# Kernel tuning notes

Hardware: AMD Instinct MI355X
Metric: run time of the kernel (lower is better)

The kernel has to match this reference:

```python
import jax, jax.numpy as jnp
import numpy as np

B, N, L = 256, 4096, 6
EMBED, HID, VOCAB = 16, 32, 200
NOTE, LSTM_D, T = 64, 64, 128


def _tree_structure():
    """One random tree of N nodes (root=node 0), tiled across the batch.
    height = distance above deepest descendant; children have strictly smaller height."""
    rng = np.random.default_rng(0)
    height = np.zeros(N, np.int32)
    height[0] = L
    height[1:] = rng.integers(0, L, N - 1)
    kind = np.full(N, 2, np.int32)  # 2 = internal
    leaf_mask = height == 0
    kind[leaf_mask] = (rng.random(leaf_mask.sum()) < 0.1).astype(np.int32)  # 1=ptr, 0=leaf
    parent = np.zeros(N, np.int64)
    for hl in range(L):
        mask = height == hl
        cand = np.where((height > hl) & (kind == 2))[0]  # root always qualifies
        parent[mask] = rng.choice(cand, size=int(mask.sum()))
    parent[0] = 0  # root points to itself; harmless (its own h stays 0 until final level)
    return height, kind, parent


def setup_inputs():
    height, kind, parent = _tree_structure()
    offs = (np.arange(B, dtype=np.int64) * N)[:, None]
    rng = np.random.default_rng(1)
    inp = {
        'kind': jnp.asarray(np.tile(kind, B), jnp.int32),
        'height': jnp.asarray(np.tile(height, B), jnp.int32),
        'parent': jnp.asarray((parent[None, :] + offs).reshape(-1), jnp.int32),
        'tok_a': jnp.asarray(rng.integers(0, VOCAB, B * N), jnp.int32),
        'tok_b': jnp.asarray(rng.integers(0, VOCAB, B * N), jnp.int32),
        'ptr_time': jnp.asarray(rng.integers(0, T, B * N), jnp.int32),
    }
    key = jax.random.key(0)
    ks = jax.random.split(key, 16)
    def w(k, shape, scale=0.05):
        return (jax.random.normal(k, shape, jnp.float32) * scale)
    inp['first_notes'] = w(ks[0], (B, NOTE), 1.0)
    inp['lstm_out'] = w(ks[1], (B, T, LSTM_D), 1.0)
    inp['embedding'] = w(ks[2], (VOCAB, EMBED), 0.02)
    inp['leaf_w1'] = w(ks[3], (2 * EMBED, HID)); inp['leaf_b1'] = w(ks[4], (HID,))
    inp['leaf_w2'] = w(ks[5], (HID, HID));       inp['leaf_b2'] = w(ks[6], (HID,))
    inp['node_w'] = w(ks[7], (2 * EMBED + HID, HID)); inp['node_b'] = w(ks[8], (HID,))
    inp['ptr_w'] = w(ks[9], (NOTE + LSTM_D, HID));    inp['ptr_b'] = w(ks[10], (HID,))
    inp['ff_w1'] = w(ks[11], (HID, HID)); inp['ff_b1'] = w(ks[12], (HID,))
    inp['ff_w2'] = w(ks[13], (HID, HID)); inp['ff_b2'] = w(ks[14], (HID,))
    inp['tail_w'] = w(ks[15], (HID, 1)); inp['tail_b'] = jnp.zeros((1,), jnp.float32)
    return inp


def reference(kind, height, parent, tok_a, tok_b, ptr_time, first_notes, lstm_out,
              embedding, leaf_w1, leaf_b1, leaf_w2, leaf_b2, node_w, node_b,
              ptr_w, ptr_b, ff_w1, ff_b1, ff_w2, ff_b2, tail_w, tail_b):
    M = kind.shape[0]
    nb = first_notes.shape[0]
    n_per = M // nb
    tree_id = jnp.arange(M, dtype=jnp.int32) // n_per
    emb_a = embedding[tok_a]  # [M, EMBED] (parent-type / first-token embed)
    emb_b = embedding[tok_b]  # [M, EMBED] (node-type / second-token embed)
    pair = jnp.concatenate([emb_a, emb_b], axis=-1)  # [M, 2*EMBED]
    # leaf path: two stacked linears (no nonlinearity), as in leaf_ff
    leaf_h = (pair @ leaf_w1 + leaf_b1) @ leaf_w2 + leaf_b2
    # ptr path: Linear(note_dim + lstm_out_dim -> hidden)
    ptr_in = jnp.concatenate([first_notes[tree_id], lstm_out[tree_id, ptr_time]], axis=-1)
    ptr_h = ptr_in @ ptr_w + ptr_b
    h = jnp.where((kind == 0)[:, None], leaf_h,
                  jnp.where((kind == 1)[:, None], ptr_h, 0.0))
    # level-synchronous child-sum: children always have smaller height
    for lvl in range(1, L + 1):
        csum = jax.ops.segment_sum(h, parent, num_segments=M)  # [M, HID]
        inner = jax.nn.relu(jnp.concatenate([pair, csum], axis=-1) @ node_w + node_b)
        h = jnp.where((height == lvl)[:, None], inner, h)
    roots = h[::n_per]  # [B, HID], root is node 0 of each tree block
    ff = (roots @ ff_w1 + ff_b1) @ ff_w2 + ff_b2
    return ff @ tail_w + tail_b  # [B, 1]


if __name__ == '__main__':
    out = reference(**setup_inputs())
    print(out.shape, out.dtype)
```

## Files before the change

### kernel.cpp

```cpp
#include <hip/hip_runtime.h>

#define BATCH   256
#define N_PER   4096
#define EMBED   16
#define HID     32
#define NOTE    64
#define LSTM_D  64
#define T_LEN   128
#define VOCAB   200
#define HSTR    (BATCH * HID)

#define MH_C0    0
#define MH_C1    1
#define MH_CNT   2
#define MH_P     7
#define MH_PBASE 8
#define OFF_K0N   64
#define OFF_K0S   (OFF_K0N + N_PER)
#define OFF_K1N   (OFF_K0S + N_PER)
#define OFF_K1S   (OFF_K1N + N_PER)
#define OFF_PLIST (OFF_K1S + N_PER)
#define OFF_WSLOT (OFF_PLIST + N_PER)
#define OFF_COFF  (OFF_WSLOT + N_PER)
#define EAW_OFF     (1024 * 1024)
#define EBW_OFF     (EAW_OFF + VOCAB * HID * 4)
#define LA2_OFF     (EBW_OFF + VOCAB * HID * 4)
#define LB2_OFF     (LA2_OFF + VOCAB * HID * 4)
#define CC_OFF      (LB2_OFF + VOCAB * HID * 4)
#define H_OFF       (8ull * 1024 * 1024)

__device__ __forceinline__ unsigned long long shflup64(unsigned long long x, int off) {
    unsigned lo = (unsigned)(x & 0xffffffffull);
    unsigned hi = (unsigned)(x >> 32);
    lo = __shfl_up(lo, off, 64);
    hi = __shfl_up(hi, off, 64);
    return ((unsigned long long)hi << 32) | (unsigned long long)lo;
}

__global__ __launch_bounds__(1024) void build_structure(
    const int* __restrict__ kind, const int* __restrict__ height,
    const int* __restrict__ parent, int* __restrict__ meta,
    const float* __restrict__ embedding,
    const float* __restrict__ leaf_w1, const float* __restrict__ leaf_b1,
    const float* __restrict__ leaf_w2, const float* __restrict__ leaf_b2,
    const float* __restrict__ node_w,
    float* __restrict__ eaw_g, float* __restrict__ ebw_g,
    float* __restrict__ la2, float* __restrict__ lb2, float* __restrict__ cc)
{
    __shared__ unsigned long long wlo[16], whi[16];
    __shared__ int wint[16];
    __shared__ int node2pidx[N_PER];
    __shared__ int deg[N_PER];
    __shared__ int sbases[8];
    __shared__ int stot[8];

    int t  = threadIdx.x;
    int i0 = 4 * t;
    int laneid = t & 63;
    int wid    = t >> 6;

    int myb[4];
    #pragma unroll
    for (int q = 0; q < 4; ++q) {
        int i = i0 + q;
        int hgt = height[i];
        int b;
        if (hgt > 0) { b = 1 + hgt; if (b > 7) b = 7; }
        else b = (kind[i] == 0) ? 0 : 1;
        myb[q] = b;
    }
    unsigned long long clo = 0, chi = 0;
    #pragma unroll
    for (int q = 0; q < 4; ++q) {
        int b = myb[q];
        if (b < 4) clo += 1ull << (16 * b);
        else       chi += 1ull << (16 * (b - 4));
    }

    unsigned long long a = clo, b64 = chi;
    #pragma unroll
    for (int off = 1; off < 64; off <<= 1) {
        unsigned long long ua = shflup64(a, off);
        unsigned long long ub = shflup64(b64, off);
        if (laneid >= off) { a += ua; b64 += ub; }
    }
    if (laneid == 63) { wlo[wid] = a; whi[wid] = b64; }
    __syncthreads();
    unsigned long long blo = 0, bhi = 0;
    for (int w = 0; w < wid; ++w) { blo += wlo[w]; bhi += whi[w]; }
    unsigned long long inc_lo = a + blo, inc_hi = b64 + bhi;
    if (t == 0) {
        unsigned long long tlo = 0, thi = 0;
        for (int w = 0; w < 16; ++w) { tlo += wlo[w]; thi += whi[w]; }
        stot[0] = (int)(tlo & 0xFFFF);         stot[1] = (int)((tlo >> 16) & 0xFFFF);
        stot[2] = (int)((tlo >> 32) & 0xFFFF); stot[3] = (int)((tlo >> 48) & 0xFFFF);
        stot[4] = (int)(thi & 0xFFFF);         stot[5] = (int)((thi >> 16) & 0xFFFF);
        stot[6] = (int)((thi >> 32) & 0xFFFF); stot[7] = (int)((thi >> 48) & 0xFFFF);
        int s = 0;
        for (int bb = 0; bb < 8; ++bb) { sbases[bb] = s; s += stot[bb]; }
        meta[MH_C0] = stot[0];
        meta[MH_C1] = stot[1];
        for (int l = 0; l < 5; ++l) meta[MH_CNT + l]   = stot[2 + l];
        for (int l = 0; l < 5; ++l) meta[MH_PBASE + l] = sbases[2 + l] - sbases[2];
        meta[MH_P] = (sbases[7] - sbases[2]) + stot[7];
    }
    __syncthreads();

    unsigned long long exlo = inc_lo - clo, exhi = inc_hi - chi;
    int mypos[4], mypidx[4];
    #pragma unroll
    for (int q = 0; q < 4; ++q) {
        int i = i0 + q, b = myb[q];
        int pos;
        if (b < 4) { pos = (int)((exlo >> (16 * b)) & 0xFFFF); exlo += 1ull << (16 * b); }
        else       { pos = (int)((exhi >> (16 * (b - 4))) & 0xFFFF); exhi += 1ull << (16 * (b - 4)); }
        mypos[q] = pos;
        int pidx = -1;
        if (b == 0)      meta[OFF_K0N + pos] = i;
        else if (b == 1) meta[OFF_K1N + pos] = i;
        else {
            pidx = (sbases[b] - sbases[2]) + pos;
            meta[OFF_PLIST + pidx] = i;
            node2pidx[i] = pidx;
        }
        mypidx[q] = pidx;
    }
    #pragma unroll
    for (int q = 0; q < 4; ++q) deg[i0 + q] = 0;
    __syncthreads();

    int par[4];
    #pragma unroll
    for (int q = 0; q < 4; ++q) {
        int i = i0 + q; par[q] = parent[i];
        if (i != 0) atomicAdd(&deg[node2pidx[par[q]]], 1);
    }
    __syncthreads();

    int d0 = deg[i0], d1 = deg[i0 + 1], d2 = deg[i0 + 2], d3 = deg[i0 + 3];
    int s4 = d0 + d1 + d2 + d3;

    int vi = s4;
    #pragma unroll
    for (int off = 1; off < 64; off <<= 1) {
        int u = __shfl_up(vi, off, 64);
        if (laneid >= off) vi += u;
    }
    if (laneid == 63) wint[wid] = vi;
    __syncthreads();
    int bint = 0;
    for (int w = 0; w < wid; ++w) bint += wint[w];
    int incl = vi + bint;

    int ex = incl - s4;
    int o0 = ex, o1 = ex + d0, o2 = o1 + d1, o3 = o2 + d2;
    deg[i0] = o0; deg[i0 + 1] = o1; deg[i0 + 2] = o2; deg[i0 + 3] = o3;
    meta[OFF_COFF + i0]     = o0;
    meta[OFF_COFF + i0 + 1] = o1;
    meta[OFF_COFF + i0 + 2] = o2;
    meta[OFF_COFF + i0 + 3] = o3;
    if (t == 1023) meta[OFF_COFF + N_PER] = o3 + d3;
    __syncthreads();

    #pragma unroll
    for (int q = 0; q < 4; ++q) {
        int i = i0 + q; if (i == 0) continue;
        int slot = atomicAdd(&deg[node2pidx[par[q]]], 1);
        int b = myb[q];
        if (b == 0)      meta[OFF_K0S + mypos[q]] = slot;
        else if (b == 1) meta[OFF_K1S + mypos[q]] = slot;
        else             meta[OFF_WSLOT + mypidx[q]] = slot;
    }

    {
        int hw = t >> 5, ln = t & 31;
        for (int v = hw; v < VOCAB; v += 32) {
            const float* ev = embedding + v * EMBED;
            float ea = 0.f, eb = 0.f, t1a = 0.f, t1b = 0.f;
            #pragma unroll
            for (int k = 0; k < EMBED; ++k) {
                float e = ev[k];
                ea  += e * node_w[k * HID + ln];
                eb  += e * node_w[(EMBED + k) * HID + ln];
                t1a += e * leaf_w1[k * HID + ln];
                t1b += e * leaf_w1[(EMBED + k) * HID + ln];
            }
            eaw_g[v * HID + ln] = ea;
            ebw_g[v * HID + ln] = eb;
            float a2 = 0.f, b2v = 0.f;
            #pragma unroll
            for (int k = 0; k < HID; ++k) {
                float w2 = leaf_w2[k * HID + ln];
                a2  += __shfl(t1a, k, 32) * w2;
                b2v += __shfl(t1b, k, 32) * w2;
            }
            la2[v * HID + ln] = a2;
            lb2[v * HID + ln] = b2v;
        }
        if (t < HID) {
            float c = leaf_b2[t];
            #pragma unroll
            for (int k = 0; k < HID; ++k) c += leaf_b1[k] * leaf_w2[k * HID + t];
            cc[t] = c;
        }
    }
}

__global__ __launch_bounds__(256) void leaf_kernel(
    const int* __restrict__ meta,
    const int* __restrict__ tok_a, const int* __restrict__ tok_b,
    const float* __restrict__ la2, const float* __restrict__ lb2,
    const float* __restrict__ cc,
    float* __restrict__ h)
{
    int lane = threadIdx.x & 31;
    int gid  = (blockIdx.x * blockDim.x + threadIdx.x) >> 5;
    int ngr  = (gridDim.x * blockDim.x) >> 5;

    float ccv = cc[lane];
    int c0 = meta[MH_C0];
    const int* K0N = meta + OFF_K0N;
    const int* K0S = meta + OFF_K0S;
    int tot = c0 * BATCH;

    for (int base = gid * 4; base < tot; base += ngr * 4) {
        int nq = tot - base; if (nq > 4) nq = 4;
        int ta[4], tb[4], slot[4], tree[4];
        #pragma unroll
        for (int q = 0; q < 4; ++q) {
            int i = base + (q < nq ? q : 0);
            int j = i >> 8; tree[q] = i & 255;
            int nd = K0N[j]; slot[q] = K0S[j];
            int gn = tree[q] * N_PER + nd;
            ta[q] = tok_a[gn]; tb[q] = tok_b[gn];
        }
        #pragma unroll
        for (int q = 0; q < 4; ++q) {
            if (q >= nq) break;
            h[(size_t)slot[q] * HSTR + tree[q] * HID + lane] =
                ccv + la2[ta[q] * HID + lane] + lb2[tb[q] * HID + lane];
        }
    }
}

__global__ __launch_bounds__(256) void ptr_kernel(
    const int* __restrict__ meta, const int* __restrict__ ptr_time,
    const float* __restrict__ first_notes, const float* __restrict__ lstm_out,
    const float* __restrict__ ptr_w, const float* __restrict__ ptr_b,
    float* __restrict__ h)
{
    int lane = threadIdx.x & 31;
    int gid  = (blockIdx.x * blockDim.x + threadIdx.x) >> 5;
    int ngr  = (gridDim.x * blockDim.x) >> 5;

    float pb = ptr_b[lane];
    int c1 = meta[MH_C1];
    const int* K1N = meta + OFF_K1N;
    const int* K1S = meta + OFF_K1S;
    int tot = c1 * BATCH;

    for (int i = gid; i < tot; i += ngr) {
        int j = i >> 8, tree = i & 255;
        int node = K1N[j], slot = K1S[j];
        int gn = tree * N_PER + node;
        int tt = ptr_time[gn];
        const float* fn = first_notes + (size_t)tree * NOTE;
        const float* lo = lstm_out + ((size_t)tree * T_LEN + tt) * LSTM_D;
        float v = pb;
        #pragma unroll
        for (int k = 0; k < NOTE; ++k)   v += fn[k] * ptr_w[k * HID + lane];
        #pragma unroll
        for (int k = 0; k < LSTM_D; ++k) v += lo[k] * ptr_w[(NOTE + k) * HID + lane];
        h[(size_t)slot * HSTR + tree * HID + lane] = v;
    }
}

__global__ __launch_bounds__(256) void level_kernel(
    const int* __restrict__ meta,
    const int* __restrict__ tok_a, const int* __restrict__ tok_b,
    const float* __restrict__ eaw_g, const float* __restrict__ ebw_g,
    const float* __restrict__ node_w, const float* __restrict__ node_b,
    float* __restrict__ h, int lvl)
{
    int cnt = meta[MH_CNT + lvl];
    if (cnt == 0) return;
    int pb  = meta[MH_PBASE + lvl];
    const int* PL = meta + OFF_PLIST;
    const int* WS = meta + OFF_WSLOT;
    const int* CO = meta + OFF_COFF;

    int lane = threadIdx.x & 31;
    int gid  = (blockIdx.x * blockDim.x + threadIdx.x) >> 5;
    int ngr  = (gridDim.x * blockDim.x) >> 5;

    float wc[HID];
    #pragma unroll
    for (int k = 0; k < HID; ++k) wc[k] = node_w[(2 * EMBED + k) * HID + lane];
    float nb = node_b[lane];

    int perchunk = cnt << 5;
    int tot = cnt * BATCH;

    for (int base = gid * 4; base < tot; base += ngr * 4) {
        int nq = tot - base; if (nq > 4) nq = 4;
        int pidx[4], tree[4];
        #pragma unroll
        for (int q = 0; q < 4; ++q) {
            int i = base + (q < nq ? q : 0);
            int tchunk = i / perchunk;
            int r = i - tchunk * perchunk;
            tree[q] = (tchunk << 5) + (r & 31);
            pidx[q] = pb + (r >> 5);
        }
        int node[4], wsl[4], e0[4], e1[4];
        #pragma unroll
        for (int q = 0; q < 4; ++q) {
            node[q] = PL[pidx[q]]; wsl[q] = WS[pidx[q]];
            e0[q] = CO[pidx[q]];  e1[q] = CO[pidx[q] + 1];
        }
        int ta[4], tb[4];
        #pragma unroll
        for (int q = 0; q < 4; ++q) {
            int gn = tree[q] * N_PER + node[q];
            ta[q] = tok_a[gn]; tb[q] = tok_b[gn];
        }
        float cs[4] = {0.f, 0.f, 0.f, 0.f};
        if (nq == 4 && pidx[0] == pidx[3]) {
            const float* hb = h + (size_t)tree[0] * HID + lane;
            int en = e1[0];
            for (int c = e0[0]; c < en; ++c) {
                size_t o = (size_t)c * HSTR;
                cs[0] += hb[o];
                cs[1] += hb[o + HID];
                cs[2] += hb[o + 2 * HID];
                cs[3] += hb[o + 3 * HID];
            }
        } else {
            #pragma unroll
            for (int q = 0; q < 4; ++q) {
                if (q >= nq) break;
                const float* hb = h + (size_t)tree[q] * HID + lane;
                float s = 0.f;
                for (int c = e0[q]; c < e1[q]; ++c) s += hb[(size_t)c * HSTR];
                cs[q] = s;
            }
        }
        #pragma unroll
        for (int q = 0; q < 4; ++q) {
            if (q >= nq) break;
            float v = nb + eaw_g[ta[q] * HID + lane] + ebw_g[tb[q] * HID + lane];
            #pragma unroll
            for (int k = 0; k < HID; ++k) v += __shfl(cs[q], k, 32) * wc[k];
            v = fmaxf(v, 0.f);
            h[(size_t)wsl[q] * HSTR + tree[q] * HID + lane] = v;
        }
    }
}

__global__ __launch_bounds__(512) void root_final_kernel(
    const int* __restrict__ meta,
    const int* __restrict__ tok_a, const int* __restrict__ tok_b,
    const float* __restrict__ eaw_g, const float* __restrict__ ebw_g,
    const float* __restrict__ h,
    const float* __restrict__ node_w, const float* __restrict__ node_b,
    const float* __restrict__ ff_w1, const float* __restrict__ ff_b1,
    const float* __restrict__ ff_w2, const float* __restrict__ ff_b2,
    const float* __restrict__ tail_w, const float* __restrict__ tail_b,
    float* __restrict__ out)
{
    __shared__ float part[16][33];
    int tree = blockIdx.x;
    int lane = threadIdx.x & 31;
    int g    = threadIdx.x >> 5;

    const int* CO = meta + OFF_COFF;
    int P = meta[MH_P];
    int e = CO[P - 1], e1 = CO[P];

    const float* hb = h + (size_t)tree * HID + lane;
    float s = 0.f;
    for (int c = e + g; c < e1; c += 16)
        s += hb[(size_t)c * HSTR];
    part[g][lane] = s;
    __syncthreads();

    if (g == 0) {
        float csum = part[0][lane];
        #pragma unroll
        for (int k = 1; k < 16; ++k) csum += part[k][lane];

        int gn = tree * N_PER;
        int ta = tok_a[gn], tb = tok_b[gn];
        float v = node_b[lane] + eaw_g[ta * HID + lane] + ebw_g[tb * HID + lane];
        #pragma unroll
        for (int k = 0; k < HID; ++k)
            v += __shfl(csum, k, 32) * node_w[(2 * EMBED + k) * HID + lane];
        v = fmaxf(v, 0.f);

        float f1 = ff_b1[lane];
        #pragma unroll
        for (int k = 0; k < HID; ++k) f1 += __shfl(v, k, 32) * ff_w1[k * HID + lane];
        float f2 = ff_b2[lane];
        #pragma unroll
        for (int k = 0; k < HID; ++k) f2 += __shfl(f1, k, 32) * ff_w2[k * HID + lane];

        float c2 = f2 * tail_w[lane];
        #pragma unroll
        for (int off = 16; off > 0; off >>= 1) c2 += __shfl_down(c2, off, 32);
        if (lane == 0) out[tree] = c2 + tail_b[0];
    }
}

extern "C" void kernel_launch(void* const* d_in, const int* in_sizes, int n_in,
                              void* d_out, int out_size, void* d_ws, size_t ws_size,
                              hipStream_t stream) {
    const int*   kind        = (const int*)d_in[0];
    const int*   height      = (const int*)d_in[1];
    const int*   parent      = (const int*)d_in[2];
    const int*   tok_a       = (const int*)d_in[3];
    const int*   tok_b       = (const int*)d_in[4];
    const int*   ptr_time    = (const int*)d_in[5];
    const float* first_notes = (const float*)d_in[6];
    const float* lstm_out    = (const float*)d_in[7];
    const float* embedding   = (const float*)d_in[8];
    const float* leaf_w1     = (const float*)d_in[9];
    const float* leaf_b1     = (const float*)d_in[10];
    const float* leaf_w2     = (const float*)d_in[11];
    const float* leaf_b2     = (const float*)d_in[12];
    const float* node_w      = (const float*)d_in[13];
    const float* node_b      = (const float*)d_in[14];
    const float* ptr_w       = (const float*)d_in[15];
    const float* ptr_b       = (const float*)d_in[16];
    const float* ff_w1       = (const float*)d_in[17];
    const float* ff_b1       = (const float*)d_in[18];
    const float* ff_w2       = (const float*)d_in[19];
    const float* ff_b2       = (const float*)d_in[20];
    const float* tail_w      = (const float*)d_in[21];
    const float* tail_b      = (const float*)d_in[22];

    char* ws = (char*)d_ws;
    int*   meta    = (int*)ws;
    float* eaw_g   = (float*)(ws + EAW_OFF);
    float* ebw_g   = (float*)(ws + EBW_OFF);
    float* la2     = (float*)(ws + LA2_OFF);
    float* lb2     = (float*)(ws + LB2_OFF);
    float* cc      = (float*)(ws + CC_OFF);
    float* h       = (float*)(ws + H_OFF);

    build_structure<<<1, 1024, 0, stream>>>(
        kind, height, parent, meta,
        embedding, leaf_w1, leaf_b1, leaf_w2, leaf_b2, node_w,
        eaw_g, ebw_g, la2, lb2, cc);

    leaf_kernel<<<2048, 256, 0, stream>>>(
        meta, tok_a, tok_b, la2, lb2, cc, h);

    ptr_kernel<<<512, 256, 0, stream>>>(
        meta, ptr_time, first_notes, lstm_out, ptr_w, ptr_b, h);

    for (int lvl = 0; lvl < 5; ++lvl) {
        level_kernel<<<2048, 256, 0, stream>>>(
            meta, tok_a, tok_b, eaw_g, ebw_g, node_w, node_b, h, lvl);
    }

    root_final_kernel<<<BATCH, 512, 0, stream>>>(
        meta, tok_a, tok_b, eaw_g, ebw_g, h, node_w, node_b,
        ff_w1, ff_b1, ff_w2, ff_b2, tail_w, tail_b, (float*)d_out);
}
```

Before: 401.2 us.

## Process eight trees per wavefront group and stage weights in LDS

Result: no change. 407.8 us (+1.6%).

```diff
diff --git a/kernel.cpp b/kernel.cpp
--- a/kernel.cpp
+++ b/kernel.cpp
@@ -59,14 +59,21 @@
     int laneid = t & 63;
     int wid    = t >> 6;
 
+    int par[4], hgt4[4], kn4[4];
+    #pragma unroll
+    for (int q = 0; q < 4; ++q) {
+        par[q]  = parent[i0 + q];
+        hgt4[q] = height[i0 + q];
+        kn4[q]  = kind[i0 + q];
+    }
+
     int myb[4];
     #pragma unroll
     for (int q = 0; q < 4; ++q) {
-        int i = i0 + q;
-        int hgt = height[i];
+        int hgt = hgt4[q];
         int b;
         if (hgt > 0) { b = 1 + hgt; if (b > 7) b = 7; }
-        else b = (kind[i] == 0) ? 0 : 1;
+        else b = (kn4[q] == 0) ? 0 : 1;
         myb[q] = b;
     }
     unsigned long long clo = 0, chi = 0;
@@ -129,10 +136,9 @@
     for (int q = 0; q < 4; ++q) deg[i0 + q] = 0;
     __syncthreads();
 
-    int par[4];
-    #pragma unroll
-    for (int q = 0; q < 4; ++q) {
-        int i = i0 + q; par[q] = parent[i];
+    #pragma unroll
+    for (int q = 0; q < 4; ++q) {
+        int i = i0 + q;
         if (i != 0) atomicAdd(&deg[node2pidx[par[q]]], 1);
     }
     __syncthreads();
@@ -223,23 +229,20 @@
     const int* K0S = meta + OFF_K0S;
     int tot = c0 * BATCH;
 
-    for (int base = gid * 4; base < tot; base += ngr * 4) {
-        int nq = tot - base; if (nq > 4) nq = 4;
-        int ta[4], tb[4], slot[4], tree[4];
-        #pragma unroll
-        for (int q = 0; q < 4; ++q) {
-            int i = base + (q < nq ? q : 0);
-            int j = i >> 8; tree[q] = i & 255;
-            int nd = K0N[j]; slot[q] = K0S[j];
-            int gn = tree[q] * N_PER + nd;
-            ta[q] = tok_a[gn]; tb[q] = tok_b[gn];
-        }
-        #pragma unroll
-        for (int q = 0; q < 4; ++q) {
-            if (q >= nq) break;
-            h[(size_t)slot[q] * HSTR + tree[q] * HID + lane] =
-                ccv + la2[ta[q] * HID + lane] + lb2[tb[q] * HID + lane];
-        }
+    for (int base = gid * 8; base < tot; base += ngr * 8) {
+        int j = base >> 8, tree0 = base & 255;
+        int nd = K0N[j], slot = K0S[j];
+        int gnb = tree0 * N_PER + nd;
+        int ta[8], tb[8];
+        #pragma unroll
+        for (int q = 0; q < 8; ++q) {
+            ta[q] = tok_a[gnb + q * N_PER];
+            tb[q] = tok_b[gnb + q * N_PER];
+        }
+        float* ob = h + (size_t)slot * HSTR + (size_t)tree0 * HID + lane;
+        #pragma unroll
+        for (int q = 0; q < 8; ++q)
+            ob[q * HID] = ccv + la2[ta[q] * HID + lane] + lb2[tb[q] * HID + lane];
     }
 }
 
@@ -249,6 +252,11 @@
     const float* __restrict__ ptr_w, const float* __restrict__ ptr_b,
     float* __restrict__ h)
 {
+    __shared__ float pw[(NOTE + LSTM_D) * HID];
+    for (int x = threadIdx.x; x < (NOTE + LSTM_D) * HID; x += 256)
+        pw[x] = ptr_w[x];
+    __syncthreads();
+
     int lane = threadIdx.x & 31;
     int gid  = (blockIdx.x * blockDim.x + threadIdx.x) >> 5;
     int ngr  = (gridDim.x * blockDim.x) >> 5;
@@ -268,9 +276,9 @@
         const float* lo = lstm_out + ((size_t)tree * T_LEN + tt) * LSTM_D;
         float v = pb;
         #pragma unroll
-        for (int k = 0; k < NOTE; ++k)   v += fn[k] * ptr_w[k * HID + lane];
-        #pragma unroll
-        for (int k = 0; k < LSTM_D; ++k) v += lo[k] * ptr_w[(NOTE + k) * HID + lane];
+        for (int k = 0; k < NOTE; ++k)   v += fn[k] * pw[k * HID + lane];
+        #pragma unroll
+        for (int k = 0; k < LSTM_D; ++k) v += lo[k] * pw[(NOTE + k) * HID + lane];
         h[(size_t)slot * HSTR + tree * HID + lane] = v;
     }
 }
@@ -282,6 +290,11 @@
     const float* __restrict__ node_w, const float* __restrict__ node_b,
     float* __restrict__ h, int lvl)
 {
+    __shared__ float wlds[HID * HID];
+    for (int x = threadIdx.x; x < HID * HID; x += 256)
+        wlds[x] = node_w[2 * EMBED * HID + x];
+    __syncthreads();
+
     int cnt = meta[MH_CNT + lvl];
     if (cnt == 0) return;
     int pb  = meta[MH_PBASE + lvl];
@@ -293,67 +306,52 @@
     int gid  = (blockIdx.x * blockDim.x + threadIdx.x) >> 5;
     int ngr  = (gridDim.x * blockDim.x) >> 5;
 
-    float wc[HID];
-    #pragma unroll
-    for (int k = 0; k < HID; ++k) wc[k] = node_w[(2 * EMBED + k) * HID + lane];
     float nb = node_b[lane];
-
     int perchunk = cnt << 5;
     int tot = cnt * BATCH;
 
-    for (int base = gid * 4; base < tot; base += ngr * 4) {
-        int nq = tot - base; if (nq > 4) nq = 4;
-        int pidx[4], tree[4];
-        #pragma unroll
-        for (int q = 0; q < 4; ++q) {
-            int i = base + (q < nq ? q : 0);
-            int tchunk = i / perchunk;
-            int r = i - tchunk * perchunk;
-            tree[q] = (tchunk << 5) + (r & 31);
-            pidx[q] = pb + (r >> 5);
-        }
-        int node[4], wsl[4], e0[4], e1[4];
-        #pragma unroll
-        for (int q = 0; q < 4; ++q) {
-            node[q] = PL[pidx[q]]; wsl[q] = WS[pidx[q]];
-            e0[q] = CO[pidx[q]];  e1[q] = CO[pidx[q] + 1];
-        }
-        int ta[4], tb[4];
-        #pragma unroll
-        for (int q = 0; q < 4; ++q) {
-            int gn = tree[q] * N_PER + node[q];
-            ta[q] = tok_a[gn]; tb[q] = tok_b[gn];
-        }
-        float cs[4] = {0.f, 0.f, 0.f, 0.f};
-        if (nq == 4 && pidx[0] == pidx[3]) {
-            const float* hb = h + (size_t)tree[0] * HID + lane;
-            int en = e1[0];
-            for (int c = e0[0]; c < en; ++c) {
-                size_t o = (size_t)c * HSTR;
-                cs[0] += hb[o];
-                cs[1] += hb[o + HID];
-                cs[2] += hb[o + 2 * HID];
-                cs[3] += hb[o + 3 * HID];
-            }
-        } else {
+    for (int base = gid * 8; base < tot; base += ngr * 8) {
+        int tchunk = base / perchunk;
+        int r      = base - tchunk * perchunk;
+        int tree0  = (tchunk << 5) + (r & 31);
+        int pidx   = pb + (r >> 5);
+
+        int node = PL[pidx], wslot = WS[pidx];
+        int e0 = CO[pidx], e1 = CO[pidx + 1];
+
+        int gnb = tree0 * N_PER + node;
+        int ta[8], tb[8];
+        #pragma unroll
+        for (int q = 0; q < 8; ++q) {
+            ta[q] = tok_a[gnb + q * N_PER];
+            tb[q] = tok_b[gnb + q * N_PER];
+        }
+
+        float cs[8] = {0.f,0.f,0.f,0.f,0.f,0.f,0.f,0.f};
+        const float* hb = h + (size_t)tree0 * HID + lane;
+        for (int c = e0; c < e1; ++c) {
+            const float* p = hb + (size_t)c * HSTR;
             #pragma unroll
-            for (int q = 0; q < 4; ++q) {
-                if (q >= nq) break;
-                const float* hb = h + (size_t)tree[q] * HID + lane;
-                float s = 0.f;
-                for (int c = e0[q]; c < e1[q]; ++c) s += hb[(size_t)c * HSTR];
-                cs[q] = s;
-            }
-        }
-        #pragma unroll
-        for (int q = 0; q < 4; ++q) {
-            if (q >= nq) break;
-            float v = nb + eaw_g[ta[q] * HID + lane] + ebw_g[tb[q] * HID + lane];
+            for (int q = 0; q < 8; ++q) cs[q] += p[q * HID];
+        }
+
+        float v[8];
+        #pragma unroll
+        for (int q = 0; q < 8; ++q)
+            v[q] = nb + eaw_g[ta[q] * HID + lane] + ebw_g[tb[q] * HID + lane];
+
+        #pragma unroll
+        for (int k = 0; k < HID; ++k) {
+            float w = wlds[k * HID + lane];
             #pragma unroll
-            for (int k = 0; k < HID; ++k) v += __shfl(cs[q], k, 32) * wc[k];
-            v = fmaxf(v, 0.f);
-            h[(size_t)wsl[q] * HSTR + tree[q] * HID + lane] = v;
-        }
+            for (int q = 0; q < 8; ++q)
+                v[q] += __shfl(cs[q], k, 32) * w;
+        }
+
+        float* ob = h + (size_t)wslot * HSTR + (size_t)tree0 * HID + lane;
+        #pragma unroll
+        for (int q = 0; q < 8; ++q)
+            ob[q * HID] = fmaxf(v[q], 0.f);
     }
 }
 
@@ -455,11 +453,11 @@
     leaf_kernel<<<2048, 256, 0, stream>>>(
         meta, tok_a, tok_b, la2, lb2, cc, h);
 
-    ptr_kernel<<<512, 256, 0, stream>>>(
+    ptr_kernel<<<1024, 256, 0, stream>>>(
         meta, ptr_time, first_notes, lstm_out, ptr_w, ptr_b, h);
 
     for (int lvl = 0; lvl < 5; ++lvl) {
-        level_kernel<<<2048, 256, 0, stream>>>(
+        level_kernel<<<1024, 256, 0, stream>>>(
             meta, tok_a, tok_b, eaw_g, ebw_g, node_w, node_b, h, lvl);
     }
 
```
